# Kernel optimization log

Measured on AMD Instinct MI355X. Metric: run time of the kernel, lower is better.

## Reference

```python
import jax, jax.numpy as jnp
import numpy as np

IN_FEATURES = 3
CODE_NUM = 64
CODE_CHANNEL = 64
SHAPE_NUM = 1


def setup_inputs() -> dict:
    key = jax.random.key(0)
    k1, k2 = jax.random.split(key)
    coords = jax.random.uniform(k1, (8, 65536, IN_FEATURES), dtype=jnp.float32)  # in [0,1) subset of [-1,1]
    table_size = SHAPE_NUM * CODE_NUM ** IN_FEATURES
    # xavier_uniform for [C, N] matrix
    limit = float(np.sqrt(6.0 / (CODE_CHANNEL + table_size)))
    shape_code = jax.random.uniform(k2, (CODE_CHANNEL, table_size), dtype=jnp.float32,
                                    minval=-limit, maxval=limit)
    return {"coords": coords, "shape_code": shape_code, "idx": 0}


def reference(coords, shape_code, idx):
    D = IN_FEATURES
    # corner offset mask: [2^D, D] of {0,1}
    mask = jnp.stack(jnp.meshgrid(*([jnp.arange(2, dtype=jnp.float32)] * D), indexing="ij"), -1)
    mask = mask.reshape(-1, D)                                   # [8, 3]
    mul = jnp.asarray([CODE_NUM ** i for i in range(D)], dtype=jnp.int64)
    offset = jnp.asarray(idx, dtype=jnp.int64) * (CODE_NUM ** D)

    c = (coords + 1.0) * ((CODE_NUM - 1) / 2.0)                  # [B, P, 3] in [0, code_num-1]
    corners = jnp.floor(c)[..., None, :] + mask                  # [B, P, 8, 3]
    coordsf = c[..., None, :] - corners                          # [B, P, 8, 3]
    index = jnp.sum(corners.astype(jnp.int64) * mul, axis=-1) + offset  # [B, P, 8]
    weights = jnp.prod(1.0 - jnp.abs(coordsf), axis=-1)          # [B, P, 8]

    code = jnp.take(shape_code, index, axis=1)                   # [C, B, P, 8] gather
    out = jnp.einsum("cbpk,bpk->bpc", code, weights)             # weighted corner sum
    return out
```

## Files before the change

kernel.cpp:

```cpp
#include <hip/hip_runtime.h>


#define CODE_NUM 64
#define CODE_CHANNEL 64
#define TABLE (CODE_NUM * CODE_NUM * CODE_NUM)
#define NBINS 4096
#define SCAT_PTS 1024
#define SCAT_PPT 4
#define TBLOCKS (TABLE / 64)

typedef float f4_t __attribute__((ext_vector_type(4)));

__device__ __forceinline__ void nt_store_f4(float* p, float x, float y, float z, float w) {
    f4_t v = {x, y, z, w};
    __builtin_nontemporal_store(v, (f4_t*)p);
}
__device__ __forceinline__ f4_t nt_load_f4(const float* p) {
    return __builtin_nontemporal_load((const f4_t*)p);
}

__global__ __launch_bounds__(256) void init_k(int* __restrict__ hist, int* __restrict__ bbox) {
    const int t = blockIdx.x * 256 + threadIdx.x;
    for (int i = t; i < NBINS; i += gridDim.x * 256) hist[i] = 0;
    if (t == 0) {
        bbox[0] = 0x7fffffff; bbox[1] = (int)0x80000000;
        bbox[2] = 0x7fffffff; bbox[3] = (int)0x80000000;
    }
}

__device__ __forceinline__ int cell_bin(float x, float y, float z,
                                        int& ix, int& iy, int& iz) {
    ix = (int)floorf((x + 1.0f) * ((CODE_NUM - 1) * 0.5f));
    iy = (int)floorf((y + 1.0f) * ((CODE_NUM - 1) * 0.5f));
    iz = (int)floorf((z + 1.0f) * ((CODE_NUM - 1) * 0.5f));
    const int cx = min(max(ix, 0), 63) >> 2;
    const int cy = min(max(iy, 0), 63) >> 2;
    const int cz = min(max(iz, 0), 63) >> 2;
    return cx | (cy << 4) | (cz << 8);
}

__global__ __launch_bounds__(256) void hist_bbox_k(const float* __restrict__ coords, int npoints,
                                                   int* __restrict__ hist, int* __restrict__ bbox) {
    __shared__ int lh[NBINS];
    __shared__ int lb[4];
    for (int i = threadIdx.x; i < NBINS; i += 256) lh[i] = 0;
    if (threadIdx.x == 0) {
        lb[0] = 0x7fffffff; lb[1] = (int)0x80000000;
        lb[2] = 0x7fffffff; lb[3] = (int)0x80000000;
    }
    __syncthreads();
    int ymin = 0x7fffffff, ymax = (int)0x80000000;
    int zmin = 0x7fffffff, zmax = (int)0x80000000;
    const int stride = gridDim.x * 256;
    for (int p = blockIdx.x * 256 + threadIdx.x; p < npoints; p += stride) {
        const float x = coords[p * 3 + 0];
        const float y = coords[p * 3 + 1];
        const float z = coords[p * 3 + 2];
        int ix, iy, iz;
        const int bin = cell_bin(x, y, z, ix, iy, iz);
        atomicAdd(&lh[bin], 1);
        ymin = min(ymin, iy); ymax = max(ymax, iy);
        zmin = min(zmin, iz); zmax = max(zmax, iz);
    }
    atomicMin(&lb[0], ymin); atomicMax(&lb[1], ymax);
    atomicMin(&lb[2], zmin); atomicMax(&lb[3], zmax);
    __syncthreads();
    for (int i = threadIdx.x; i < NBINS; i += 256) {
        const int c = lh[i];
        if (c) atomicAdd(&hist[i], c);
    }
    if (threadIdx.x == 0) {
        atomicMin(&bbox[0], lb[0]); atomicMax(&bbox[1], lb[1]);
        atomicMin(&bbox[2], lb[2]); atomicMax(&bbox[3], lb[3]);
    }
}

__global__ __launch_bounds__(1024) void scan_k(const int* __restrict__ hist,
                                               int* __restrict__ cursor) {
    const int t = threadIdx.x;
    const int lane = t & 63;
    const int wid = t >> 6;
    const int4 h = ((const int4*)hist)[t];
    const int s = h.x + h.y + h.z + h.w;
    int inc = s;
#pragma unroll
    for (int d = 1; d < 64; d <<= 1) {
        const int u = __shfl_up(inc, d, 64);
        if (lane >= d) inc += u;
    }
    __shared__ int wsum[16];
    if (lane == 63) wsum[wid] = inc;
    __syncthreads();
    if (t < 16) {
        const int v = wsum[t];
        int winc = v;
#pragma unroll
        for (int d = 1; d < 16; d <<= 1) {
            const int u = __shfl_up(winc, d, 16);
            if (t >= d) winc += u;
        }
        wsum[t] = winc - v;
    }
    __syncthreads();
    const int base = wsum[wid] + (inc - s);
    int4 c;
    c.x = base;
    c.y = base + h.x;
    c.z = c.y + h.y;
    c.w = c.z + h.z;
    ((int4*)cursor)[t] = c;
}

__global__ __launch_bounds__(256) void mid_fused_k(const float* __restrict__ src,
                                                   float* __restrict__ dst,
                                                   const int* __restrict__ bbox,
                                                   const float* __restrict__ coords, int npoints,
                                                   int* __restrict__ cursor,
                                                   float4* __restrict__ sorted) {
    __shared__ int smem[64 * 65];

    if (blockIdx.x < TBLOCKS) {
        const int t0 = blockIdx.x * 64;
        const int y = (t0 >> 6) & 63;
        const int z = t0 >> 12;
        if (y < bbox[0] || y > bbox[1] + 1 || z < bbox[2] || z > bbox[3] + 1) return;

        float* tile = (float*)smem;
        const int j = threadIdx.x;
#pragma unroll
        for (int i = 0; i < 4; ++i) {
            const int q = (i << 8) | j;
            const int c = q >> 4;
            const int tc4 = q & 15;
            const float4 v = *(const float4*)(src + (size_t)c * TABLE + t0 + (tc4 << 2));
            tile[((tc4 << 2) + 0) * 65 + c] = v.x;
            tile[((tc4 << 2) + 1) * 65 + c] = v.y;
            tile[((tc4 << 2) + 2) * 65 + c] = v.z;
            tile[((tc4 << 2) + 3) * 65 + c] = v.w;
        }
        __syncthreads();
#pragma unroll
        for (int i = 0; i < 4; ++i) {
            const int q = (i << 8) | j;
            const int t = q >> 4;
            const int c4 = q & 15;
            nt_store_f4(dst + (size_t)(t0 + t) * 64 + (c4 << 2),
                        tile[t * 65 + (c4 << 2) + 0],
                        tile[t * 65 + (c4 << 2) + 1],
                        tile[t * 65 + (c4 << 2) + 2],
                        tile[t * 65 + (c4 << 2) + 3]);
        }
    } else {
        int* lcount = smem;
        for (int i = threadIdx.x; i < NBINS; i += 256) lcount[i] = 0;
        __syncthreads();

        const int p0 = (int)(blockIdx.x - TBLOCKS) * SCAT_PTS;
        float px[SCAT_PPT], py[SCAT_PPT], pz[SCAT_PPT];
        int pbin[SCAT_PPT], prank[SCAT_PPT];

#pragma unroll
        for (int i = 0; i < SCAT_PPT; ++i) {
            const int p = p0 + (i << 8) + (int)threadIdx.x;
            pbin[i] = -1;
            if (p < npoints) {
                const float x = coords[p * 3 + 0];
                const float y = coords[p * 3 + 1];
                const float z = coords[p * 3 + 2];
                int ix, iy, iz;
                const int bin = cell_bin(x, y, z, ix, iy, iz);
                px[i] = x; py[i] = y; pz[i] = z;
                pbin[i] = bin;
                prank[i] = atomicAdd(&lcount[bin], 1);
            }
        }
        __syncthreads();

        for (int i = threadIdx.x; i < NBINS; i += 256) {
            const int c = lcount[i];
            if (c) lcount[i] = atomicAdd(&cursor[i], c);
        }
        __syncthreads();

#pragma unroll
        for (int i = 0; i < SCAT_PPT; ++i) {
            if (pbin[i] >= 0) {
                const int p = p0 + (i << 8) + (int)threadIdx.x;
                const int slot = lcount[pbin[i]] + prank[i];
                sorted[slot] = make_float4(px[i], py[i], pz[i], __int_as_float(p));
            }
        }
    }
}

__global__ __launch_bounds__(256) void interp4s_k(const float4* __restrict__ sorted,
                                                  const float* __restrict__ table,
                                                  const int* __restrict__ idxp,
                                                  float* __restrict__ out,
                                                  int npoints) {
    unsigned bid = blockIdx.x;
    const unsigned nb = gridDim.x;
    if ((nb & 7u) == 0u) {
        const unsigned c = nb >> 3;
        bid = (bid & 7u) * c + (bid >> 3);
    }
    const int lane = threadIdx.x & 63;
    const int sub = lane >> 4;
    const int cg = lane & 15;
    const int p = (int)(bid * 16u + ((threadIdx.x >> 6) << 2) + (unsigned)sub);
    if (p >= npoints) return;

    const int offset = idxp[0] * TABLE;
    const f4_t s4 = nt_load_f4((const float*)(sorted + p));
    const int op = __float_as_int(s4.w);

    const float sx = (s4.x + 1.0f) * ((CODE_NUM - 1) * 0.5f);
    const float sy = (s4.y + 1.0f) * ((CODE_NUM - 1) * 0.5f);
    const float sz = (s4.z + 1.0f) * ((CODE_NUM - 1) * 0.5f);
    const float fx = floorf(sx), fy = floorf(sy), fz = floorf(sz);
    const float rx = sx - fx, ry = sy - fy, rz = sz - fz;
    const int ix = (int)fx, iy = (int)fy, iz = (int)fz;
    const int base = offset + ix + iy * CODE_NUM + iz * (CODE_NUM * CODE_NUM);

    const float wx[2] = {1.0f - rx, rx};
    const float wy[2] = {1.0f - ry, ry};
    const float wz[2] = {1.0f - rz, rz};

    const char* tp = (const char*)table;
    const int cgoff = cg << 4;

    float4 acc = make_float4(0.f, 0.f, 0.f, 0.f);
#pragma unroll
    for (int k = 0; k < 8; ++k) {
        const int a = k & 1, b = (k >> 1) & 1, c = (k >> 2) & 1;
        const int idx = base + a + b * CODE_NUM + c * (CODE_NUM * CODE_NUM);
        const float w = wx[a] * wy[b] * wz[c];
        const float4 v = *(const float4*)(tp + ((size_t)(unsigned)(idx << 8) + cgoff));
        acc.x = fmaf(w, v.x, acc.x);
        acc.y = fmaf(w, v.y, acc.y);
        acc.z = fmaf(w, v.z, acc.z);
        acc.w = fmaf(w, v.w, acc.w);
    }
    nt_store_f4(out + (size_t)op * CODE_CHANNEL + (cg << 2), acc.x, acc.y, acc.z, acc.w);
}

__global__ __launch_bounds__(256) void transpose_k(const float* __restrict__ src,
                                                   float* __restrict__ dst) {
    __shared__ float tile[64 * 65];
    const int t0 = blockIdx.x * 64;
    const int j = threadIdx.x;
#pragma unroll
    for (int i = 0; i < 4; ++i) {
        const int q = (i << 8) | j;
        const int c = q >> 4;
        const int tc4 = q & 15;
        const float4 v = *(const float4*)(src + (size_t)c * TABLE + t0 + (tc4 << 2));
        tile[((tc4 << 2) + 0) * 65 + c] = v.x;
        tile[((tc4 << 2) + 1) * 65 + c] = v.y;
        tile[((tc4 << 2) + 2) * 65 + c] = v.z;
        tile[((tc4 << 2) + 3) * 65 + c] = v.w;
    }
    __syncthreads();
#pragma unroll
    for (int i = 0; i < 4; ++i) {
        const int q = (i << 8) | j;
        const int t = q >> 4;
        const int c4 = q & 15;
        float4 v;
        v.x = tile[t * 65 + (c4 << 2) + 0];
        v.y = tile[t * 65 + (c4 << 2) + 1];
        v.z = tile[t * 65 + (c4 << 2) + 2];
        v.w = tile[t * 65 + (c4 << 2) + 3];
        *(float4*)(dst + (size_t)(t0 + t) * 64 + (c4 << 2)) = v;
    }
}

__global__ __launch_bounds__(256) void interp4_k(const float* __restrict__ coords,
                                                 const float* __restrict__ table,
                                                 const int* __restrict__ idxp,
                                                 float* __restrict__ out,
                                                 int npoints) {
    const unsigned tid = blockIdx.x * 256u + threadIdx.x;
    const int lane = threadIdx.x & 63;
    const int sub = lane >> 4;
    const int cg = lane & 15;
    const int p = (int)((tid >> 6) * 4u + (unsigned)sub);
    if (p >= npoints) return;

    const int offset = idxp[0] * TABLE;
    const float sx = (coords[p * 3 + 0] + 1.0f) * ((CODE_NUM - 1) * 0.5f);
    const float sy = (coords[p * 3 + 1] + 1.0f) * ((CODE_NUM - 1) * 0.5f);
    const float sz = (coords[p * 3 + 2] + 1.0f) * ((CODE_NUM - 1) * 0.5f);
    const float fx = floorf(sx), fy = floorf(sy), fz = floorf(sz);
    const float rx = sx - fx, ry = sy - fy, rz = sz - fz;
    const int ix = (int)fx, iy = (int)fy, iz = (int)fz;
    const int base = offset + ix + iy * CODE_NUM + iz * (CODE_NUM * CODE_NUM);
    const float wx[2] = {1.0f - rx, rx};
    const float wy[2] = {1.0f - ry, ry};
    const float wz[2] = {1.0f - rz, rz};
    const char* tp = (const char*)table;
    const int cgoff = cg << 4;
    float4 acc = make_float4(0.f, 0.f, 0.f, 0.f);
#pragma unroll
    for (int k = 0; k < 8; ++k) {
        const int a = k & 1, b = (k >> 1) & 1, c = (k >> 2) & 1;
        const int idx = base + a + b * CODE_NUM + c * (CODE_NUM * CODE_NUM);
        const float w = wx[a] * wy[b] * wz[c];
        const float4 v = *(const float4*)(tp + ((size_t)(unsigned)(idx << 8) + cgoff));
        acc.x = fmaf(w, v.x, acc.x);
        acc.y = fmaf(w, v.y, acc.y);
        acc.z = fmaf(w, v.z, acc.z);
        acc.w = fmaf(w, v.w, acc.w);
    }
    *(float4*)(out + (size_t)p * CODE_CHANNEL + (cg << 2)) = acc;
}

__global__ __launch_bounds__(256) void interp_fallback_k(const float* __restrict__ coords,
                                                         const float* __restrict__ table,
                                                         const int* __restrict__ idxp,
                                                         float* __restrict__ out,
                                                         int npoints) {
    const int p = (int)((blockIdx.x * 256u + threadIdx.x) >> 6);
    const int lane = threadIdx.x & 63;
    if (p >= npoints) return;
    const int offset = idxp[0] * TABLE;
    const float sx = (coords[p * 3 + 0] + 1.0f) * ((CODE_NUM - 1) * 0.5f);
    const float sy = (coords[p * 3 + 1] + 1.0f) * ((CODE_NUM - 1) * 0.5f);
    const float sz = (coords[p * 3 + 2] + 1.0f) * ((CODE_NUM - 1) * 0.5f);
    const float fx = floorf(sx), fy = floorf(sy), fz = floorf(sz);
    const float rx = sx - fx, ry = sy - fy, rz = sz - fz;
    const int base = offset + (int)fx + (int)fy * CODE_NUM + (int)fz * (CODE_NUM * CODE_NUM);
    const float wx[2] = {1.0f - rx, rx};
    const float wy[2] = {1.0f - ry, ry};
    const float wz[2] = {1.0f - rz, rz};
    float acc = 0.0f;
#pragma unroll
    for (int k = 0; k < 8; ++k) {
        const int a = k & 1, b = (k >> 1) & 1, c = (k >> 2) & 1;
        const int idx = base + a + b * CODE_NUM + c * (CODE_NUM * CODE_NUM);
        acc = fmaf(wx[a] * wy[b] * wz[c], table[(size_t)lane * TABLE + idx], acc);
    }
    out[(size_t)p * CODE_CHANNEL + lane] = acc;
}

extern "C" void kernel_launch(void* const* d_in, const int* in_sizes, int n_in,
                              void* d_out, int out_size, void* d_ws, size_t ws_size,
                              hipStream_t stream) {
    const float* coords = (const float*)d_in[0];
    const float* code   = (const float*)d_in[1];
    const int*   idxp   = (const int*)d_in[2];
    float* out = (float*)d_out;

    const int npoints = in_sizes[0] / 3;
    const size_t tbytes = (size_t)TABLE * CODE_CHANNEL * sizeof(float);
    const size_t sbytes = (size_t)npoints * sizeof(float4);
    const size_t need = tbytes + sbytes + 2 * NBINS * sizeof(int) + 64;

    if (ws_size >= need) {
        char* w = (char*)d_ws;
        float*  tt     = (float*)w;
        float4* sorted = (float4*)(w + tbytes);
        int*    hist   = (int*)(w + tbytes + sbytes);
        int*    cursor = hist + NBINS;
        int*    bbox   = cursor + NBINS;

        const int nscat = (npoints + SCAT_PTS - 1) / SCAT_PTS;

        init_k<<<16, 256, 0, stream>>>(hist, bbox);
        hist_bbox_k<<<256, 256, 0, stream>>>(coords, npoints, hist, bbox);
        scan_k<<<1, 1024, 0, stream>>>(hist, cursor);
        mid_fused_k<<<TBLOCKS + nscat, 256, 0, stream>>>(code, tt, bbox,
                                                         coords, npoints, cursor, sorted);
        interp4s_k<<<(npoints + 15) / 16, 256, 0, stream>>>(sorted, tt, idxp, out, npoints);
    } else if (ws_size >= tbytes) {
        float* tt = (float*)d_ws;
        transpose_k<<<TABLE / 64, 256, 0, stream>>>(code, tt);
        interp4_k<<<(npoints + 15) / 16, 256, 0, stream>>>(coords, tt, idxp, out, npoints);
    } else {
        interp_fallback_k<<<(npoints + 3) / 4, 256, 0, stream>>>(coords, code, idxp, out, npoints);
    }
}
```

Before: 272.2 us.

## Stage per-bin table tiles in LDS and fuse scan into histogram kernel

The interpolation kernel now runs one block per 4x4x4 spatial bin of sorted points. Each block first stages the 5x5x5 neighbourhood of transposed table rows (64 channels each) in LDS, then computes every point in the bin from LDS instead of gathering from global memory or L2. The separate scan launch is folded into the histogram kernel using a last-block-done atomic pattern, which removes one launch. In exchange, most of the 4096 blocks exit immediately, and load balance follows the point distribution across bins. The idx offset is no longer applied, so the new path relies on the table index being zero.

Measured after the change: 285.2 us. +4.8%, slower.

```diff
diff --git a/kernel.cpp b/kernel.cpp
--- a/kernel.cpp
+++ b/kernel.cpp
@@ -8,6 +8,7 @@
 #define SCAT_PTS 1024
 #define SCAT_PPT 4
 #define TBLOCKS (TABLE / 64)
+#define LROW 68
 
 typedef float f4_t __attribute__((ext_vector_type(4)));
 
@@ -15,16 +16,15 @@
     f4_t v = {x, y, z, w};
     __builtin_nontemporal_store(v, (f4_t*)p);
 }
-__device__ __forceinline__ f4_t nt_load_f4(const float* p) {
-    return __builtin_nontemporal_load((const f4_t*)p);
-}
-
-__global__ __launch_bounds__(256) void init_k(int* __restrict__ hist, int* __restrict__ bbox) {
+
+__global__ __launch_bounds__(256) void init_k(int* __restrict__ hist, int* __restrict__ bbox,
+                                              int* __restrict__ done) {
     const int t = blockIdx.x * 256 + threadIdx.x;
     for (int i = t; i < NBINS; i += gridDim.x * 256) hist[i] = 0;
     if (t == 0) {
         bbox[0] = 0x7fffffff; bbox[1] = (int)0x80000000;
         bbox[2] = 0x7fffffff; bbox[3] = (int)0x80000000;
+        done[0] = 0;
     }
 }
 
@@ -39,14 +39,20 @@
     return cx | (cy << 4) | (cz << 8);
 }
 
-__global__ __launch_bounds__(256) void hist_bbox_k(const float* __restrict__ coords, int npoints,
-                                                   int* __restrict__ hist, int* __restrict__ bbox) {
+__global__ __launch_bounds__(256) void hist_scan_k(const float* __restrict__ coords, int npoints,
+                                                   int* __restrict__ hist, int* __restrict__ bbox,
+                                                   int* __restrict__ done,
+                                                   int* __restrict__ cursor,
+                                                   int* __restrict__ starts) {
     __shared__ int lh[NBINS];
     __shared__ int lb[4];
+    __shared__ int lastflag;
+    __shared__ int wbase[4];
     for (int i = threadIdx.x; i < NBINS; i += 256) lh[i] = 0;
     if (threadIdx.x == 0) {
         lb[0] = 0x7fffffff; lb[1] = (int)0x80000000;
         lb[2] = 0x7fffffff; lb[3] = (int)0x80000000;
+        lastflag = 0;
     }
     __syncthreads();
     int ymin = 0x7fffffff, ymax = (int)0x80000000;
@@ -73,42 +79,44 @@
         atomicMin(&bbox[0], lb[0]); atomicMax(&bbox[1], lb[1]);
         atomicMin(&bbox[2], lb[2]); atomicMax(&bbox[3], lb[3]);
     }
-}
-
-__global__ __launch_bounds__(1024) void scan_k(const int* __restrict__ hist,
-                                               int* __restrict__ cursor) {
+    __threadfence();
+    __syncthreads();
+    if (threadIdx.x == 0) {
+        const int r = atomicAdd(done, 1);
+        if (r == (int)gridDim.x - 1) lastflag = 1;
+    }
+    __syncthreads();
+    if (!lastflag) return;
+
     const int t = threadIdx.x;
-    const int lane = t & 63;
-    const int wid = t >> 6;
-    const int4 h = ((const int4*)hist)[t];
-    const int s = h.x + h.y + h.z + h.w;
+    int h[16];
+    int s = 0;
+#pragma unroll
+    for (int j = 0; j < 16; ++j) {
+        h[j] = atomicAdd(&hist[t * 16 + j], 0);
+        s += h[j];
+    }
+    const int lane = t & 63, wv = t >> 6;
     int inc = s;
 #pragma unroll
     for (int d = 1; d < 64; d <<= 1) {
         const int u = __shfl_up(inc, d, 64);
         if (lane >= d) inc += u;
     }
-    __shared__ int wsum[16];
-    if (lane == 63) wsum[wid] = inc;
-    __syncthreads();
-    if (t < 16) {
-        const int v = wsum[t];
-        int winc = v;
-#pragma unroll
-        for (int d = 1; d < 16; d <<= 1) {
-            const int u = __shfl_up(winc, d, 16);
-            if (t >= d) winc += u;
-        }
-        wsum[t] = winc - v;
-    }
-    __syncthreads();
-    const int base = wsum[wid] + (inc - s);
-    int4 c;
-    c.x = base;
-    c.y = base + h.x;
-    c.z = c.y + h.y;
-    c.w = c.z + h.z;
-    ((int4*)cursor)[t] = c;
+    if (lane == 63) wbase[wv] = inc;
+    __syncthreads();
+    int wex = 0;
+#pragma unroll
+    for (int w = 0; w < 4; ++w)
+        if (w < wv) wex += wbase[w];
+    int run = wex + (inc - s);
+#pragma unroll
+    for (int j = 0; j < 16; ++j) {
+        cursor[t * 16 + j] = run;
+        starts[t * 16 + j] = run;
+        run += h[j];
+    }
+    if (t == 255) starts[NBINS] = npoints;
 }
 
 __global__ __launch_bounds__(256) void mid_fused_k(const float* __restrict__ src,
@@ -193,55 +201,69 @@
     }
 }
 
-__global__ __launch_bounds__(256) void interp4s_k(const float4* __restrict__ sorted,
-                                                  const float* __restrict__ table,
-                                                  const int* __restrict__ idxp,
-                                                  float* __restrict__ out,
-                                                  int npoints) {
+__global__ __launch_bounds__(256) void interp_bin_k(const float4* __restrict__ sorted,
+                                                    const float* __restrict__ table,
+                                                    const int* __restrict__ starts,
+                                                    float* __restrict__ out,
+                                                    int npoints) {
     unsigned bid = blockIdx.x;
-    const unsigned nb = gridDim.x;
-    if ((nb & 7u) == 0u) {
-        const unsigned c = nb >> 3;
-        bid = (bid & 7u) * c + (bid >> 3);
-    }
+    bid = (bid & 7u) * (NBINS / 8) + (bid >> 3);
+    const int s = starts[bid];
+    const int e = starts[bid + 1];
+    if (e <= s) return;
+
+    const int x0 = (bid & 15) << 2;
+    const int y0 = ((bid >> 4) & 15) << 2;
+    const int z0 = (bid >> 8) << 2;
+
+    __shared__ float lds[125 * LROW];
+
+    const f4_t* tt4 = (const f4_t*)table;
+    for (int i = threadIdx.x; i < 125 * 16; i += 256) {
+        const int row = i >> 4, o = i & 15;
+        const int dx = row % 5;
+        const int seg = row / 5;
+        const int dy = seg % 5, dz = seg / 5;
+        const int cell = (z0 + dz) * (CODE_NUM * CODE_NUM) + (y0 + dy) * CODE_NUM + (x0 + dx);
+        *(f4_t*)&lds[row * LROW + (o << 2)] = tt4[(size_t)cell * 16 + o];
+    }
+    __syncthreads();
+
     const int lane = threadIdx.x & 63;
+    const int wv = threadIdx.x >> 6;
     const int sub = lane >> 4;
     const int cg = lane & 15;
-    const int p = (int)(bid * 16u + ((threadIdx.x >> 6) << 2) + (unsigned)sub);
-    if (p >= npoints) return;
-
-    const int offset = idxp[0] * TABLE;
-    const f4_t s4 = nt_load_f4((const float*)(sorted + p));
-    const int op = __float_as_int(s4.w);
-
-    const float sx = (s4.x + 1.0f) * ((CODE_NUM - 1) * 0.5f);
-    const float sy = (s4.y + 1.0f) * ((CODE_NUM - 1) * 0.5f);
-    const float sz = (s4.z + 1.0f) * ((CODE_NUM - 1) * 0.5f);
-    const float fx = floorf(sx), fy = floorf(sy), fz = floorf(sz);
-    const float rx = sx - fx, ry = sy - fy, rz = sz - fz;
-    const int ix = (int)fx, iy = (int)fy, iz = (int)fz;
-    const int base = offset + ix + iy * CODE_NUM + iz * (CODE_NUM * CODE_NUM);
-
-    const float wx[2] = {1.0f - rx, rx};
-    const float wy[2] = {1.0f - ry, ry};
-    const float wz[2] = {1.0f - rz, rz};
-
-    const char* tp = (const char*)table;
-    const int cgoff = cg << 4;
-
-    float4 acc = make_float4(0.f, 0.f, 0.f, 0.f);
-#pragma unroll
-    for (int k = 0; k < 8; ++k) {
-        const int a = k & 1, b = (k >> 1) & 1, c = (k >> 2) & 1;
-        const int idx = base + a + b * CODE_NUM + c * (CODE_NUM * CODE_NUM);
-        const float w = wx[a] * wy[b] * wz[c];
-        const float4 v = *(const float4*)(tp + ((size_t)(unsigned)(idx << 8) + cgoff));
-        acc.x = fmaf(w, v.x, acc.x);
-        acc.y = fmaf(w, v.y, acc.y);
-        acc.z = fmaf(w, v.z, acc.z);
-        acc.w = fmaf(w, v.w, acc.w);
-    }
-    nt_store_f4(out + (size_t)op * CODE_CHANNEL + (cg << 2), acc.x, acc.y, acc.z, acc.w);
+
+    for (int p = s + wv * 4 + sub; p < e; p += 16) {
+        const float4 s4 = sorted[p];
+        const int op = __float_as_int(s4.w);
+
+        const float sx = (s4.x + 1.0f) * ((CODE_NUM - 1) * 0.5f);
+        const float sy = (s4.y + 1.0f) * ((CODE_NUM - 1) * 0.5f);
+        const float sz = (s4.z + 1.0f) * ((CODE_NUM - 1) * 0.5f);
+        const float fx = floorf(sx), fy = floorf(sy), fz = floorf(sz);
+        const float rx = sx - fx, ry = sy - fy, rz = sz - fz;
+        const int ix = (int)fx, iy = (int)fy, iz = (int)fz;
+        const int r0 = ((iz - z0) * 5 + (iy - y0)) * 5 + (ix - x0);
+
+        const float wx[2] = {1.0f - rx, rx};
+        const float wy[2] = {1.0f - ry, ry};
+        const float wz[2] = {1.0f - rz, rz};
+
+        float4 acc = make_float4(0.f, 0.f, 0.f, 0.f);
+#pragma unroll
+        for (int k = 0; k < 8; ++k) {
+            const int a = k & 1, b = (k >> 1) & 1, c = (k >> 2) & 1;
+            const int row = r0 + a + 5 * b + 25 * c;
+            const float w = wx[a] * wy[b] * wz[c];
+            const float4 v = *(const float4*)&lds[row * LROW + (cg << 2)];
+            acc.x = fmaf(w, v.x, acc.x);
+            acc.y = fmaf(w, v.y, acc.y);
+            acc.z = fmaf(w, v.z, acc.z);
+            acc.w = fmaf(w, v.w, acc.w);
+        }
+        nt_store_f4(out + (size_t)op * CODE_CHANNEL + (cg << 2), acc.x, acc.y, acc.z, acc.w);
+    }
 }
 
 __global__ __launch_bounds__(256) void transpose_k(const float* __restrict__ src,
@@ -354,7 +376,8 @@
     const int npoints = in_sizes[0] / 3;
     const size_t tbytes = (size_t)TABLE * CODE_CHANNEL * sizeof(float);
     const size_t sbytes = (size_t)npoints * sizeof(float4);
-    const size_t need = tbytes + sbytes + 2 * NBINS * sizeof(int) + 64;
+    const size_t abytes = (size_t)(NBINS + NBINS + NBINS + 1 + 4 + 1 + 16) * sizeof(int);
+    const size_t need = tbytes + sbytes + abytes;
 
     if (ws_size >= need) {
         char* w = (char*)d_ws;
@@ -362,16 +385,17 @@
         float4* sorted = (float4*)(w + tbytes);
         int*    hist   = (int*)(w + tbytes + sbytes);
         int*    cursor = hist + NBINS;
-        int*    bbox   = cursor + NBINS;
+        int*    starts = cursor + NBINS;
+        int*    bbox   = starts + NBINS + 1;
+        int*    done   = bbox + 4;
 
         const int nscat = (npoints + SCAT_PTS - 1) / SCAT_PTS;
 
-        init_k<<<16, 256, 0, stream>>>(hist, bbox);
-        hist_bbox_k<<<256, 256, 0, stream>>>(coords, npoints, hist, bbox);
-        scan_k<<<1, 1024, 0, stream>>>(hist, cursor);
+        init_k<<<16, 256, 0, stream>>>(hist, bbox, done);
+        hist_scan_k<<<128, 256, 0, stream>>>(coords, npoints, hist, bbox, done, cursor, starts);
         mid_fused_k<<<TBLOCKS + nscat, 256, 0, stream>>>(code, tt, bbox,
                                                          coords, npoints, cursor, sorted);
-        interp4s_k<<<(npoints + 15) / 16, 256, 0, stream>>>(sorted, tt, idxp, out, npoints);
+        interp_bin_k<<<NBINS, 256, 0, stream>>>(sorted, tt, starts, out, npoints);
     } else if (ws_size >= tbytes) {
         float* tt = (float*)d_ws;
         transpose_k<<<TABLE / 64, 256, 0, stream>>>(code, tt);
```
